# Kernel optimization log

Measured on AMD Instinct MI355X. Metric: run time of the kernel, lower is better.

The kernel has to match this reference:

```python
import jax, jax.numpy as jnp
import numpy as np

B, S, NV, D = 2, 4096, 8, 256
E = 256          # embedding dim for adaLN conditioning
H = 8            # D / n_head_channels(=32)
HID = 4 * D      # ResLayer MLP hidden
EPS = 1e-5


def setup_inputs() -> dict:
    key = jax.random.key(0)
    ks = jax.random.split(key, 16)
    M = NV * D

    def w(k, shape, scale=0.02):
        return jax.random.normal(k, shape, dtype=jnp.float32) * scale

    mask = jax.random.uniform(ks[0], (B, S, NV)) > 0.2
    mask = mask.at[..., 0].set(True)  # avoid fully-masked rows
    return {
        "x": jax.random.normal(ks[1], (B, S, NV, D), dtype=jnp.float32),
        "emb": jax.random.normal(ks[2], (B, E), dtype=jnp.float32),
        "mask": mask,
        "w_mod1": w(ks[3], (E, 2 * M)), "b_mod1": jnp.zeros((2 * M,), jnp.float32),
        "wq": w(ks[4], (D, D)), "bq": jnp.zeros((D,), jnp.float32),
        "wk": w(ks[5], (D, D)), "bk": jnp.zeros((D,), jnp.float32),
        "wv": w(ks[6], (D, D)), "bv": jnp.zeros((D,), jnp.float32),
        "wo": w(ks[7], (D, D)), "bo": jnp.zeros((D,), jnp.float32),
        "gamma": jnp.full((D,), 1e-6, jnp.float32),
        "w_mod2": w(ks[8], (E, 2 * M)), "b_mod2": jnp.zeros((2 * M,), jnp.float32),
        "w1": w(ks[9], (D, HID)), "b1": jnp.zeros((HID,), jnp.float32),
        "w2": w(ks[10], (HID, D)), "b2": jnp.zeros((D,), jnp.float32),
        "gamma_mlp": jnp.full((D,), 1e-6, jnp.float32),
    }


def _adaln(xin, emb, w, b):
    # AdaptiveLayerNorm over the flattened (NV*D) feature dims,
    # scale/shift conditioned on the embedding.
    b_, s_, nv_, d_ = xin.shape
    xf = xin.reshape(b_, s_, nv_ * d_)
    mu = xf.mean(-1, keepdims=True)
    var = ((xf - mu) ** 2).mean(-1, keepdims=True)
    normed = (xf - mu) * jax.lax.rsqrt(var + EPS)
    scale, shift = jnp.split(emb @ w + b, 2, axis=-1)  # [B, NV*D] each
    out = normed * (1.0 + scale[:, None, :]) + shift[:, None, :]
    return out.reshape(b_, s_, nv_, d_)


def reference(x, emb, mask, w_mod1, b_mod1, wq, bq, wk, bk, wv, bv, wo, bo,
              gamma, w_mod2, b_mod2, w1, b1, w2, b2, gamma_mlp):
    b_, s_, nv_, d_ = x.shape
    hd = d_ // H
    inv_sqrt = jnp.float32(1.0 / np.sqrt(hd))

    # --- attention branch: adaLN -> shape_to_att -> masked attention over variables ---
    h = _adaln(x, emb, w_mod1, b_mod1).reshape(b_ * s_, nv_, d_)
    q = (h @ wq + bq).reshape(b_ * s_, nv_, H, hd)
    k = (h @ wk + bk).reshape(b_ * s_, nv_, H, hd)
    v = (h @ wv + bv).reshape(b_ * s_, nv_, H, hd)
    scores = jnp.einsum('bnhd,bmhd->bhnm', q, k) * inv_sqrt  # [B*S, H, NV, NV]
    mk = mask.reshape(b_ * s_, nv_)
    scores = jnp.where(mk[:, None, None, :], scores, jnp.float32(-1e9))
    attn = jax.nn.softmax(scores, axis=-1)
    o = jnp.einsum('bhnm,bmhd->bnhd', attn, v).reshape(b_ * s_, nv_, d_)
    o = o @ wo + bo
    # dropout is identity at eval; gamma-scaled residual add
    x1 = x + gamma * o.reshape(b_, s_, nv_, d_)

    # --- MLP branch: shape_to_x -> adaLN -> shape_to_att -> ResLayer -> gamma residual ---
    h2 = _adaln(x1, emb, w_mod2, b_mod2)
    m = jax.nn.gelu(h2 @ w1 + b1) @ w2 + b2
    return x1 + gamma_mlp * m
```

## Files before the change

kernel.cpp:

```cpp
#include <hip/hip_runtime.h>
#include <hip/hip_bf16.h>
#include <stdint.h>

#define S_TOK   8192
#define MFEAT   2048

typedef __attribute__((ext_vector_type(4))) float f32x4;
typedef __attribute__((ext_vector_type(8))) short bf16x8;

__device__ __forceinline__ float b2f(uint32_t u) { return __uint_as_float(u << 16); }
__device__ __forceinline__ uint16_t f2b(float f) {
  uint32_t u = __float_as_uint(f);
  uint32_t r = u + 0x7fffu + ((u >> 16) & 1u);
  return (uint16_t)(r >> 16);
}

#define GLP(p) ((__attribute__((address_space(1))) void*)(uintptr_t)(p))
#define LDSP(p) ((__attribute__((address_space(3))) void*)(p))

__global__ __launch_bounds__(256) void k_maskprobe(const uint32_t* __restrict__ m,
                                                   int* __restrict__ flag) {
  __shared__ int s[5];
  const int tid = threadIdx.x;
  if (tid < 5) s[tid] = (tid == 4) ? 0 : 1;
  __syncthreads();
  bool i32ok = true, i8ok = true, f32ok = true, bf16ok = true, saw = false;
  for (int i = tid; i < 1024; i += 256) {
    uint32_t w = m[i];
    if (w > 1u) i32ok = false;
    if (((w | (w >> 8) | (w >> 16) | (w >> 24)) & 0xFEu) != 0) i8ok = false;
    if (w != 0u && w != 0x3F800000u) f32ok = false;
    uint32_t h0 = w & 0xffffu, h1 = w >> 16;
    if ((h0 != 0u && h0 != 0x3F80u) || (h1 != 0u && h1 != 0x3F80u)) bf16ok = false;
    if (w == 0x3F803F80u) saw = true;
  }
  if (!i32ok) s[0] = 0;
  if (!i8ok)  s[1] = 0;
  if (!f32ok) s[2] = 0;
  if (!bf16ok) s[3] = 0;
  if (saw)    s[4] = 1;
  __syncthreads();
  if (tid == 0) {
    int f;
    if (s[0]) f = 0;
    else if (s[1]) f = 1;
    else if (s[3] && s[4]) f = 3;
    else if (s[2]) f = 2;
    else if (s[3]) f = 3;
    else f = 0;
    *flag = f;
  }
}

__global__ __launch_bounds__(256) void k_prep(
    const float* __restrict__ wq, const float* __restrict__ wk,
    const float* __restrict__ wv, const float* __restrict__ wo,
    const float* __restrict__ w1, const float* __restrict__ w2,
    uint16_t* __restrict__ wqf, uint16_t* __restrict__ wot,
    uint16_t* __restrict__ w1f, uint16_t* __restrict__ w2f,
    const void* __restrict__ mask, const int* __restrict__ flag,
    int* __restrict__ mask_i32,
    const float* __restrict__ bq, const float* __restrict__ bk,
    const float* __restrict__ bv, float* __restrict__ biasqkv) {
  int idx = blockIdx.x * 256 + threadIdx.x;
  if (idx < 196608) {
    int o = idx, frag = o >> 9, lane = (o >> 3) & 63, sub = o & 7;
    int ct = frag >> 3, kt = frag & 7;
    int col = ct * 16 + (lane & 15);
    int k = kt * 32 + (lane >> 4) * 8 + sub;
    const float* src = (col < 256) ? wq : (col < 512) ? wk : wv;
    wqf[idx] = f2b(src[k * 256 + (col & 255)]);
  } else if (idx < 262144) {
    int r = idx - 196608;
    int k = r >> 8, n = r & 255;
    wot[n * 256 + k] = f2b(wo[r]);
  } else if (idx < 524288) {
    int o = idx - 262144, frag = o >> 9, lane = (o >> 3) & 63, sub = o & 7;
    int ct = frag >> 3, kt = frag & 7;
    int col = ct * 16 + (lane & 15);
    int k = kt * 32 + (lane >> 4) * 8 + sub;
    w1f[o] = f2b(w1[k * 1024 + col]);
  } else if (idx < 786432) {
    int o = idx - 524288, frag = o >> 9, lane = (o >> 3) & 63, sub = o & 7;
    int ct = frag >> 5, kt = frag & 31;
    int col = ct * 16 + (lane & 15);
    int k = kt * 32 + (lane >> 4) * 8 + sub;
    w2f[o] = f2b(w2[k * 256 + col]);
  } else if (idx < 851968) {
    int i = idx - 786432;
    int f = *flag;
    int v;
    if (f == 0)      v = ((const int*)mask)[i] != 0;
    else if (f == 1) v = ((const uint8_t*)mask)[i] != 0;
    else if (f == 2) v = ((const uint32_t*)mask)[i] != 0;
    else             v = ((const uint16_t*)mask)[i] != 0;
    mask_i32[i] = v;
  } else if (idx < 852736) {
    int i = idx - 851968;
    biasqkv[i] = (i < 256) ? bq[i] : (i < 512) ? bk[i - 256] : bv[i - 512];
  }
}

__global__ __launch_bounds__(256) void k_mods(
    const float* __restrict__ emb,
    const float* __restrict__ w_mod1, const float* __restrict__ b_mod1,
    const float* __restrict__ w_mod2, const float* __restrict__ b_mod2,
    float* __restrict__ mods) {
  const int j = blockIdx.x * 256 + threadIdx.x;
  const int b = blockIdx.y;
  const int which = blockIdx.z;
  const float* w  = which ? w_mod2 : w_mod1;
  const float* bb = which ? b_mod2 : b_mod1;
  __shared__ float e[256];
  e[threadIdx.x] = emb[b * 256 + threadIdx.x];
  __syncthreads();
  float acc = bb[j];
  for (int kx = 0; kx < 256; kx++) acc += e[kx] * w[(size_t)kx * 4096 + j];
  mods[((size_t)which * 2 + b) * 4096 + j] = acc;
}

__global__ __launch_bounds__(256) void k_adaln(
    const float* __restrict__ xin, const float* __restrict__ mods,
    uint16_t* __restrict__ hout, int tbase) {
  const int t = blockIdx.x;
  const int b = (tbase + t) >> 12;
  const int tid = threadIdx.x;
  const float4* xp = (const float4*)(xin + (size_t)t * MFEAT + tid * 8);
  float4 u0 = xp[0], u1 = xp[1];
  float f[8] = {u0.x, u0.y, u0.z, u0.w, u1.x, u1.y, u1.z, u1.w};
  float s1 = 0.f, s2 = 0.f;
#pragma unroll
  for (int i = 0; i < 8; i++) { s1 += f[i]; s2 += f[i] * f[i]; }
#pragma unroll
  for (int off = 32; off; off >>= 1) {
    s1 += __shfl_down(s1, off);
    s2 += __shfl_down(s2, off);
  }
  __shared__ float red[8];
  if ((tid & 63) == 0) { red[(tid >> 6) * 2] = s1; red[(tid >> 6) * 2 + 1] = s2; }
  __syncthreads();
  s1 = red[0] + red[2] + red[4] + red[6];
  s2 = red[1] + red[3] + red[5] + red[7];
  const float mean = s1 * (1.f / 2048.f);
  const float var  = s2 * (1.f / 2048.f) - mean * mean;
  const float rs = rsqrtf(var + 1e-5f);
  const float* mo = mods + (size_t)b * 4096;
  uint32_t w[4];
#pragma unroll
  for (int i = 0; i < 4; i++) {
    int j0 = tid * 8 + i * 2;
    float y0 = (f[i*2]   - mean) * rs * (1.f + mo[j0])     + mo[2048 + j0];
    float y1 = (f[i*2+1] - mean) * rs * (1.f + mo[j0 + 1]) + mo[2048 + j0 + 1];
    w[i] = (uint32_t)f2b(y0) | ((uint32_t)f2b(y1) << 16);
  }
  *(uint4*)(hout + (size_t)t * MFEAT + tid * 8) = make_uint4(w[0], w[1], w[2], w[3]);
}

template <int K, int EPI, int RESF32, int OUTF32, int SPLIT>
__global__ __launch_bounds__(256) void k_gemm(
    const uint16_t* __restrict__ A, const uint16_t* __restrict__ Wt,
    const float* __restrict__ bias, const void* res,
    const float* __restrict__ gam, void* out, int N, size_t splitStride) {
  __shared__ __align__(16) uint16_t As[128 * 64];
  __shared__ __align__(16) uint16_t Bs[128 * 64];
  const int tid = threadIdx.x;
  const int l = tid & 63;
  const int wva = tid >> 6;
  const int wr = wva >> 1, wc = wva & 1;
  const int brow = blockIdx.x * 128;
  const int bcol = blockIdx.y * 128;

  f32x4 acc[4][4];
#pragma unroll
  for (int m = 0; m < 4; m++)
#pragma unroll
    for (int n = 0; n < 4; n++) acc[m][n] = (f32x4)0.f;

  char* AsB = (char*)As;
  char* BsB = (char*)Bs;

  for (int kt = 0; kt < K / 64; ++kt) {
    const int k0 = kt * 64;
#pragma unroll
    for (int i = 0; i < 4; i++) {
      int chunk = wva * 4 + i;
      int r = chunk * 8 + (l >> 3);
      int cb = (l & 7) * 16;
      int sb = cb ^ ((r & 7) << 4);
      const uint16_t* ga = A  + (size_t)(brow + r) * K + k0 + (sb >> 1);
      const uint16_t* gb = Wt + (size_t)(bcol + r) * K + k0 + (sb >> 1);
      __builtin_amdgcn_global_load_lds(GLP(ga), LDSP(AsB + chunk * 1024), 16, 0, 0);
      __builtin_amdgcn_global_load_lds(GLP(gb), LDSP(BsB + chunk * 1024), 16, 0, 0);
    }
    asm volatile("s_waitcnt vmcnt(0)" ::: "memory");
    __syncthreads();

#pragma unroll
    for (int kk = 0; kk < 2; kk++) {
      bf16x8 a[4], b[4];
#pragma unroll
      for (int m = 0; m < 4; m++) {
        int row = wr * 64 + m * 16 + (l & 15);
        int cb = (kk * 64 + (l >> 4) * 16) ^ ((row & 7) << 4);
        a[m] = *(const bf16x8*)(AsB + row * 128 + cb);
      }
#pragma unroll
      for (int n = 0; n < 4; n++) {
        int row = wc * 64 + n * 16 + (l & 15);
        int cb = (kk * 64 + (l >> 4) * 16) ^ ((row & 7) << 4);
        b[n] = *(const bf16x8*)(BsB + row * 128 + cb);
      }
#pragma unroll
      for (int m = 0; m < 4; m++)
#pragma unroll
        for (int n = 0; n < 4; n++)
          acc[m][n] = __builtin_amdgcn_mfma_f32_16x16x32_bf16(a[m], b[n], acc[m][n], 0, 0, 0);
    }
    __syncthreads();
  }

#pragma unroll
  for (int m = 0; m < 4; m++) {
#pragma unroll
    for (int n = 0; n < 4; n++) {
      int col = bcol + wc * 64 + n * 16 + (l & 15);
      float bc = bias[col];
      float gc = (EPI == 2) ? gam[col] : 0.f;
#pragma unroll
      for (int r = 0; r < 4; r++) {
        int row = brow + wr * 64 + m * 16 + (l >> 4) * 4 + r;
        float y = acc[m][n][r] + bc;
        if (EPI == 2) {
          float rv = RESF32 ? ((const float*)res)[(size_t)row * N + col]
                            : b2f(((const uint16_t*)res)[(size_t)row * N + col]);
          y = rv + gc * y;
        }
        if (SPLIT) {
          int b_ = col >> 8, coll = col & 255;
          ((uint16_t*)out)[(size_t)b_ * splitStride + (size_t)row * 256 + coll] = f2b(y);
        } else if (OUTF32) {
          ((float*)out)[(size_t)row * N + col] = y;
        } else {
          ((uint16_t*)out)[(size_t)row * N + col] = f2b(y);
        }
      }
    }
  }
}

template <int NB>
__global__ __launch_bounds__(256) void k_panel(
    const uint16_t* __restrict__ A, const uint16_t* __restrict__ Wf,
    const float* __restrict__ bias, uint16_t* __restrict__ out,
    size_t splitStride) {
  __shared__ __align__(16) uint16_t As[128 * 256];
  const int tid = threadIdx.x;
  const int l = tid & 63;
  const int wva = tid >> 6;
  const int wr = wva >> 1, wc = wva & 1;
  const int brow = blockIdx.x * 128;
  char* AsB = (char*)As;

#pragma unroll
  for (int i = 0; i < 16; i++) {
    int chunk = wva * 16 + i;
    int r = chunk * 2 + (l >> 5);
    int sb = ((l & 31) * 16) ^ ((r & 7) << 4);
    __builtin_amdgcn_global_load_lds(GLP(A + (size_t)(brow + r) * 256 + (sb >> 1)),
                                     LDSP(AsB + chunk * 1024), 16, 0, 0);
  }
  asm volatile("s_waitcnt vmcnt(0)" ::: "memory");
  __syncthreads();

#pragma unroll 1
  for (int nb = 0; nb < NB; nb++) {
    f32x4 acc[4][4];
#pragma unroll
    for (int m = 0; m < 4; m++)
#pragma unroll
      for (int n = 0; n < 4; n++) acc[m][n] = (f32x4)0.f;

#pragma unroll
    for (int kt = 0; kt < 8; kt++) {
      bf16x8 a[4], b[4];
#pragma unroll
      for (int n = 0; n < 4; n++) {
        int ct = nb * 8 + wc * 4 + n;
        b[n] = *(const bf16x8*)(Wf + (((size_t)ct * 8 + kt) * 64 + l) * 8);
      }
#pragma unroll
      for (int m = 0; m < 4; m++) {
        int row = wr * 64 + m * 16 + (l & 15);
        int cb = (kt * 64 + (l >> 4) * 16) ^ ((row & 7) << 4);
        a[m] = *(const bf16x8*)(AsB + row * 512 + cb);
      }
#pragma unroll
      for (int m = 0; m < 4; m++)
#pragma unroll
        for (int n = 0; n < 4; n++)
          acc[m][n] = __builtin_amdgcn_mfma_f32_16x16x32_bf16(a[m], b[n], acc[m][n], 0, 0, 0);
    }

#pragma unroll
    for (int m = 0; m < 4; m++) {
#pragma unroll
      for (int n = 0; n < 4; n++) {
        int col = nb * 128 + wc * 64 + n * 16 + (l & 15);
        float bc = bias[col];
        int b_ = col >> 8, coll = col & 255;
#pragma unroll
        for (int r = 0; r < 4; r++) {
          int row = brow + wr * 64 + m * 16 + (l >> 4) * 4 + r;
          out[(size_t)b_ * splitStride + (size_t)row * 256 + coll] = f2b(acc[m][n][r] + bc);
        }
      }
    }
  }
}

__global__ __launch_bounds__(256) void k_mlp(
    const uint16_t* __restrict__ A, const uint16_t* __restrict__ w1f,
    const float* __restrict__ b1, const uint16_t* __restrict__ w2f,
    const float* __restrict__ b2, const float* __restrict__ gam,
    float* x1c) {
  __shared__ __align__(16) uint16_t As[64 * 256];
  __shared__ __align__(16) uint16_t Hs[64 * 128];
  const int tid = threadIdx.x;
  const int l = tid & 63;
  const int w = tid >> 6;
  const int brow = blockIdx.x * 64;
  char* AsB = (char*)As;
  char* HsB = (char*)Hs;

#pragma unroll
  for (int i = 0; i < 8; i++) {
    int chunk = w * 8 + i;
    int r = chunk * 2 + (l >> 5);
    int sb = ((l & 31) * 16) ^ ((r & 7) << 4);
    __builtin_amdgcn_global_load_lds(GLP(A + (size_t)(brow + r) * 256 + (sb >> 1)),
                                     LDSP(AsB + chunk * 1024), 16, 0, 0);
  }

  f32x4 acc2[4][4];
#pragma unroll
  for (int m = 0; m < 4; m++)
#pragma unroll
    for (int n = 0; n < 4; n++) acc2[m][n] = (f32x4)0.f;

  asm volatile("s_waitcnt vmcnt(0)" ::: "memory");
  __syncthreads();

#pragma unroll 1
  for (int c = 0; c < 8; c++) {
    f32x4 acc1[2][4];
#pragma unroll
    for (int n = 0; n < 2; n++)
#pragma unroll
      for (int m = 0; m < 4; m++) acc1[n][m] = (f32x4)0.f;
#pragma unroll
    for (int kt = 0; kt < 8; kt++) {
      bf16x8 a[4], b[2];
#pragma unroll
      for (int n = 0; n < 2; n++) {
        int ct = c * 8 + w * 2 + n;
        b[n] = *(const bf16x8*)(w1f + (((size_t)ct * 8 + kt) * 64 + l) * 8);
      }
#pragma unroll
      for (int m = 0; m < 4; m++) {
        int row = m * 16 + (l & 15);
        int cb = (kt * 64 + (l >> 4) * 16) ^ ((row & 7) << 4);
        a[m] = *(const bf16x8*)(AsB + row * 512 + cb);
      }
#pragma unroll
      for (int n = 0; n < 2; n++)
#pragma unroll
        for (int m = 0; m < 4; m++)
          acc1[n][m] = __builtin_amdgcn_mfma_f32_16x16x32_bf16(b[n], a[m], acc1[n][m], 0, 0, 0);
    }
    __syncthreads();
#pragma unroll
    for (int n = 0; n < 2; n++) {
      int hb = w * 32 + n * 16 + (l >> 4) * 4;
      float4 bb = *(const float4*)(b1 + c * 128 + hb);
#pragma unroll
      for (int m = 0; m < 4; m++) {
        int token = m * 16 + (l & 15);
        uint32_t pk[2];
#pragma unroll
        for (int h = 0; h < 2; h++) {
          float g[2];
#pragma unroll
          for (int j = 0; j < 2; j++) {
            float y = acc1[n][m][h * 2 + j] + ((const float*)&bb)[h * 2 + j];
            g[j] = y / (1.f + __expf(-1.702f * y));
          }
          pk[h] = (uint32_t)f2b(g[0]) | ((uint32_t)f2b(g[1]) << 16);
        }
        int byte = (token * 256 + hb * 2) ^ ((token & 7) << 4);
        *(uint2*)(HsB + byte) = make_uint2(pk[0], pk[1]);
      }
    }
    __syncthreads();
#pragma unroll
    for (int kt = 0; kt < 4; kt++) {
      bf16x8 h[4], b[4];
#pragma unroll
      for (int n = 0; n < 4; n++) {
        int ct = w * 4 + n;
        int kidx = c * 4 + kt;
        b[n] = *(const bf16x8*)(w2f + (((size_t)ct * 32 + kidx) * 64 + l) * 8);
      }
#pragma unroll
      for (int m = 0; m < 4; m++) {
        int row = m * 16 + (l & 15);
        int cb = (kt * 64 + (l >> 4) * 16) ^ ((row & 7) << 4);
        h[m] = *(const bf16x8*)(HsB + row * 256 + cb);
      }
#pragma unroll
      for (int m = 0; m < 4; m++)
#pragma unroll
        for (int n = 0; n < 4; n++)
          acc2[m][n] = __builtin_amdgcn_mfma_f32_16x16x32_bf16(h[m], b[n], acc2[m][n], 0, 0, 0);
    }
  }

#pragma unroll
  for (int m = 0; m < 4; m++) {
#pragma unroll
    for (int n = 0; n < 4; n++) {
      int col = w * 64 + n * 16 + (l & 15);
      float bc = b2[col];
      float gc = gam[col];
#pragma unroll
      for (int r = 0; r < 4; r++) {
        int row = brow + m * 16 + (l >> 4) * 4 + r;
        float y = x1c[(size_t)row * 256 + col] + gc * (acc2[m][n][r] + bc);
        x1c[(size_t)row * 256 + col] = y;
      }
    }
  }
}

__global__ __launch_bounds__(256) void k_attn(
    const uint16_t* __restrict__ q, const uint16_t* __restrict__ k,
    const uint16_t* __restrict__ v, const int* __restrict__ mask,
    uint16_t* __restrict__ o) {
  __shared__ __align__(16) uint16_t kk[4][2048];
  __shared__ __align__(16) uint16_t vv[4][2048];
  const int l = threadIdx.x & 63;
  const int wva = threadIdx.x >> 6;
  const int t = blockIdx.x * 4 + wva;

#pragma unroll
  for (int c = 0; c < 4; c++) {
    __builtin_amdgcn_global_load_lds(GLP(k + (size_t)t * 2048 + c * 512 + l * 8),
                                     LDSP(&kk[wva][c * 512]), 16, 0, 0);
    __builtin_amdgcn_global_load_lds(GLP(v + (size_t)t * 2048 + c * 512 + l * 8),
                                     LDSP(&vv[wva][c * 512]), 16, 0, 0);
  }

  const int h = l >> 3, n = l & 7;
  const uint4* qp = (const uint4*)(q + (size_t)t * 2048 + n * 256 + h * 32);
  float qf[32];
#pragma unroll
  for (int c = 0; c < 4; c++) {
    uint4 u = qp[c];
    qf[c*8+0]=b2f(u.x & 0xffff); qf[c*8+1]=b2f(u.x >> 16);
    qf[c*8+2]=b2f(u.y & 0xffff); qf[c*8+3]=b2f(u.y >> 16);
    qf[c*8+4]=b2f(u.z & 0xffff); qf[c*8+5]=b2f(u.z >> 16);
    qf[c*8+6]=b2f(u.w & 0xffff); qf[c*8+7]=b2f(u.w >> 16);
  }
  asm volatile("s_waitcnt vmcnt(0)" ::: "memory");

  float s[8];
#pragma unroll
  for (int m = 0; m < 8; m++) {
    const uint4* kp = (const uint4*)&kk[wva][m * 256 + h * 32];
    float acc = 0.f;
#pragma unroll
    for (int c = 0; c < 4; c++) {
      uint4 u = kp[c];
      acc += qf[c*8+0]*b2f(u.x & 0xffff) + qf[c*8+1]*b2f(u.x >> 16)
           + qf[c*8+2]*b2f(u.y & 0xffff) + qf[c*8+3]*b2f(u.y >> 16)
           + qf[c*8+4]*b2f(u.z & 0xffff) + qf[c*8+5]*b2f(u.z >> 16)
           + qf[c*8+6]*b2f(u.w & 0xffff) + qf[c*8+7]*b2f(u.w >> 16);
    }
    s[m] = acc * 0.17677669529663687f;
  }
  const int* mk = mask + (size_t)t * 8;
  float mx = -1e30f;
#pragma unroll
  for (int m = 0; m < 8; m++) { s[m] = mk[m] ? s[m] : -1e9f; mx = fmaxf(mx, s[m]); }
  float p[8], sum = 0.f;
#pragma unroll
  for (int m = 0; m < 8; m++) { p[m] = __expf(s[m] - mx); sum += p[m]; }
  float inv = 1.f / sum;
  float of[32];
#pragma unroll
  for (int d = 0; d < 32; d++) of[d] = 0.f;
#pragma unroll
  for (int m = 0; m < 8; m++) {
    float pm = p[m] * inv;
    const uint4* vp = (const uint4*)&vv[wva][m * 256 + h * 32];
#pragma unroll
    for (int c = 0; c < 4; c++) {
      uint4 u = vp[c];
      of[c*8+0]+=pm*b2f(u.x & 0xffff); of[c*8+1]+=pm*b2f(u.x >> 16);
      of[c*8+2]+=pm*b2f(u.y & 0xffff); of[c*8+3]+=pm*b2f(u.y >> 16);
      of[c*8+4]+=pm*b2f(u.z & 0xffff); of[c*8+5]+=pm*b2f(u.z >> 16);
      of[c*8+6]+=pm*b2f(u.w & 0xffff); of[c*8+7]+=pm*b2f(u.w >> 16);
    }
  }
  uint16_t* op = o + (size_t)t * 2048 + n * 256 + h * 32;
#pragma unroll
  for (int c = 0; c < 4; c++) {
    uint32_t w0 = (uint32_t)f2b(of[c*8+0]) | ((uint32_t)f2b(of[c*8+1]) << 16);
    uint32_t w1 = (uint32_t)f2b(of[c*8+2]) | ((uint32_t)f2b(of[c*8+3]) << 16);
    uint32_t w2 = (uint32_t)f2b(of[c*8+4]) | ((uint32_t)f2b(of[c*8+5]) << 16);
    uint32_t w3 = (uint32_t)f2b(of[c*8+6]) | ((uint32_t)f2b(of[c*8+7]) << 16);
    ((uint4*)op)[c] = make_uint4(w0, w1, w2, w3);
  }
}

extern "C" void kernel_launch(void* const* d_in, const int* in_sizes, int n_in,
                              void* d_out, int out_size, void* d_ws, size_t ws_size,
                              hipStream_t stream) {
  const float* x      = (const float*)d_in[0];
  const float* emb    = (const float*)d_in[1];
  const void*  mask   = d_in[2];
  const float* w_mod1 = (const float*)d_in[3];
  const float* b_mod1 = (const float*)d_in[4];
  const float* wq = (const float*)d_in[5];
  const float* bq = (const float*)d_in[6];
  const float* wk = (const float*)d_in[7];
  const float* bk = (const float*)d_in[8];
  const float* wv = (const float*)d_in[9];
  const float* bv = (const float*)d_in[10];
  const float* wo = (const float*)d_in[11];
  const float* bo = (const float*)d_in[12];
  const float* gamma     = (const float*)d_in[13];
  const float* w_mod2    = (const float*)d_in[14];
  const float* b_mod2    = (const float*)d_in[15];
  const float* w1 = (const float*)d_in[16];
  const float* b1 = (const float*)d_in[17];
  const float* w2 = (const float*)d_in[18];
  const float* b2 = (const float*)d_in[19];
  const float* gamma_mlp = (const float*)d_in[20];

  char* ws = (char*)d_ws;
  float*    mods = (float*)ws;
  uint16_t* wqf = (uint16_t*)(ws + 65536);
  uint16_t* wot = wqf + 196608;
  uint16_t* w1f = wot + 65536;
  uint16_t* w2f = w1f + 262144;
  int*      mask_i32 = (int*)(w2f + 262144);
  int*      flag = mask_i32 + 65536;
  float*    biasqkv = (float*)(flag + 1);
  uint16_t* slots = (uint16_t*)(ws + (2u << 20));
  float*    xout = (float*)d_out;

  size_t budget = (ws_size > (3u << 20)) ? ws_size - (2u << 20) : 0;
  int maxtok = (int)(budget / 16384);
  int chunk_tokens = 16;
  for (int c = 8192; c >= 16; c >>= 1) { if (c <= maxtok) { chunk_tokens = c; break; } }
  const int nchunks = S_TOK / chunk_tokens;
  const int crows = chunk_tokens * 8;
  const size_t slot = (size_t)crows * 256;
  uint16_t* C0 = slots;
  uint16_t* C1 = C0 + slot;

  k_maskprobe<<<dim3(1), 256, 0, stream>>>((const uint32_t*)mask, flag);
  k_prep<<<dim3(3331), 256, 0, stream>>>(wq, wk, wv, wo, w1, w2, wqf, wot, w1f, w2f,
                                         mask, flag, mask_i32, bq, bk, bv, biasqkv);
  k_mods<<<dim3(16, 2, 2), 256, 0, stream>>>(emb, w_mod1, b_mod1, w_mod2, b_mod2, mods);

  for (int c = 0; c < nchunks; c++) {
    const int t0 = c * chunk_tokens;
    const size_t eo = (size_t)t0 * MFEAT;
    const float* xc = x + eo;
    float* x1c = xout + eo;
    k_adaln<<<dim3(chunk_tokens), 256, 0, stream>>>(xc, mods, C0, t0);
    k_panel<6><<<dim3(crows / 128), 256, 0, stream>>>(C0, wqf, biasqkv, C1, slot);
    k_attn<<<dim3(chunk_tokens / 4), 256, 0, stream>>>(C1, C1 + slot, C1 + 2 * slot,
                                                       mask_i32 + (size_t)t0 * 8, C0);
    k_gemm<256, 2, 1, 1, 0><<<dim3(crows / 128, 2), 256, 0, stream>>>(
        C0, wot, bo, xc, gamma, x1c, 256, 0);
    k_adaln<<<dim3(chunk_tokens), 256, 0, stream>>>(x1c, mods + 2 * 4096, C0, t0);
    k_mlp<<<dim3(crows / 64), 256, 0, stream>>>(C0, w1f, b1, w2f, b2, gamma_mlp, x1c);
  }
}
```

Measured before the change: 335.6 us.

## Fuse adaLN into QKV and MLP GEMMs, convert o-proj to fragment-layout panel

Removes the two standalone adaLN kernels by computing per-token mean/variance and the modulated normalization inside the QKV projection and MLP kernels, writing bf16 directly into LDS. This cuts the intermediate bf16 activation round-trip through global memory and two launches per chunk. The output projection switches from a tiled LDS GEMM with transposed weights to a panel kernel reading pre-fragmented weights. The cost is that x rows are read twice inside each fused kernel (once for stats, once for normalization), and the extra reductions add shared-memory work.

```diff
diff --git a/kernel.cpp b/kernel.cpp
--- a/kernel.cpp
+++ b/kernel.cpp
@@ -56,7 +56,7 @@
     const float* __restrict__ wq, const float* __restrict__ wk,
     const float* __restrict__ wv, const float* __restrict__ wo,
     const float* __restrict__ w1, const float* __restrict__ w2,
-    uint16_t* __restrict__ wqf, uint16_t* __restrict__ wot,
+    uint16_t* __restrict__ wqf, uint16_t* __restrict__ wof,
     uint16_t* __restrict__ w1f, uint16_t* __restrict__ w2f,
     const void* __restrict__ mask, const int* __restrict__ flag,
     int* __restrict__ mask_i32,
@@ -71,9 +71,11 @@
     const float* src = (col < 256) ? wq : (col < 512) ? wk : wv;
     wqf[idx] = f2b(src[k * 256 + (col & 255)]);
   } else if (idx < 262144) {
-    int r = idx - 196608;
-    int k = r >> 8, n = r & 255;
-    wot[n * 256 + k] = f2b(wo[r]);
+    int o = idx - 196608, frag = o >> 9, lane = (o >> 3) & 63, sub = o & 7;
+    int ct = frag >> 3, kt = frag & 7;
+    int col = ct * 16 + (lane & 15);
+    int k = kt * 32 + (lane >> 4) * 8 + sub;
+    wof[o] = f2b(wo[k * 256 + col]);
   } else if (idx < 524288) {
     int o = idx - 262144, frag = o >> 9, lane = (o >> 3) & 63, sub = o & 7;
     int ct = frag >> 3, kt = frag & 7;
@@ -119,96 +121,93 @@
   mods[((size_t)which * 2 + b) * 4096 + j] = acc;
 }
 
-__global__ __launch_bounds__(256) void k_adaln(
-    const float* __restrict__ xin, const float* __restrict__ mods,
-    uint16_t* __restrict__ hout, int tbase) {
-  const int t = blockIdx.x;
-  const int b = (tbase + t) >> 12;
-  const int tid = threadIdx.x;
-  const float4* xp = (const float4*)(xin + (size_t)t * MFEAT + tid * 8);
-  float4 u0 = xp[0], u1 = xp[1];
-  float f[8] = {u0.x, u0.y, u0.z, u0.w, u1.x, u1.y, u1.z, u1.w};
-  float s1 = 0.f, s2 = 0.f;
-#pragma unroll
-  for (int i = 0; i < 8; i++) { s1 += f[i]; s2 += f[i] * f[i]; }
-#pragma unroll
-  for (int off = 32; off; off >>= 1) {
-    s1 += __shfl_down(s1, off);
-    s2 += __shfl_down(s2, off);
-  }
-  __shared__ float red[8];
-  if ((tid & 63) == 0) { red[(tid >> 6) * 2] = s1; red[(tid >> 6) * 2 + 1] = s2; }
-  __syncthreads();
-  s1 = red[0] + red[2] + red[4] + red[6];
-  s2 = red[1] + red[3] + red[5] + red[7];
-  const float mean = s1 * (1.f / 2048.f);
-  const float var  = s2 * (1.f / 2048.f) - mean * mean;
-  const float rs = rsqrtf(var + 1e-5f);
-  const float* mo = mods + (size_t)b * 4096;
-  uint32_t w[4];
-#pragma unroll
-  for (int i = 0; i < 4; i++) {
-    int j0 = tid * 8 + i * 2;
-    float y0 = (f[i*2]   - mean) * rs * (1.f + mo[j0])     + mo[2048 + j0];
-    float y1 = (f[i*2+1] - mean) * rs * (1.f + mo[j0 + 1]) + mo[2048 + j0 + 1];
-    w[i] = (uint32_t)f2b(y0) | ((uint32_t)f2b(y1) << 16);
-  }
-  *(uint4*)(hout + (size_t)t * MFEAT + tid * 8) = make_uint4(w[0], w[1], w[2], w[3]);
-}
-
-template <int K, int EPI, int RESF32, int OUTF32, int SPLIT>
-__global__ __launch_bounds__(256) void k_gemm(
-    const uint16_t* __restrict__ A, const uint16_t* __restrict__ Wt,
-    const float* __restrict__ bias, const void* res,
-    const float* __restrict__ gam, void* out, int N, size_t splitStride) {
-  __shared__ __align__(16) uint16_t As[128 * 64];
-  __shared__ __align__(16) uint16_t Bs[128 * 64];
+__global__ __launch_bounds__(256) void k_qkv(
+    const float* __restrict__ x, const float* __restrict__ mods,
+    const float* __restrict__ biasqkv, const uint16_t* __restrict__ wqf,
+    uint16_t* __restrict__ out, size_t slot, int t0) {
+  __shared__ __align__(16) uint16_t As[128 * 256];
+  __shared__ float red1[256], red2[256];
   const int tid = threadIdx.x;
   const int l = tid & 63;
   const int wva = tid >> 6;
   const int wr = wva >> 1, wc = wva & 1;
   const int brow = blockIdx.x * 128;
-  const int bcol = blockIdx.y * 128;
-
-  f32x4 acc[4][4];
-#pragma unroll
-  for (int m = 0; m < 4; m++)
-#pragma unroll
-    for (int n = 0; n < 4; n++) acc[m][n] = (f32x4)0.f;
-
   char* AsB = (char*)As;
-  char* BsB = (char*)Bs;
-
-  for (int kt = 0; kt < K / 64; ++kt) {
-    const int k0 = kt * 64;
+
+  {
+    const int r = tid >> 1, ch = (tid & 1) << 7;
+    const float4* xp = (const float4*)(x + (size_t)(brow + r) * 256 + ch);
+    float s1 = 0.f, s2 = 0.f;
+#pragma unroll
+    for (int i = 0; i < 32; i++) {
+      float4 u = xp[i];
+      s1 += u.x + u.y + u.z + u.w;
+      s2 += u.x * u.x + u.y * u.y + u.z * u.z + u.w * u.w;
+    }
+    red1[tid] = s1; red2[tid] = s2;
+  }
+  __syncthreads();
+  {
+    const int r = tid >> 1;
+    const int base = (r >> 3) << 4;
+    float s1 = 0.f, s2 = 0.f;
+#pragma unroll
+    for (int i = 0; i < 16; i++) { s1 += red1[base + i]; s2 += red2[base + i]; }
+    float mean = s1 * (1.f / 2048.f);
+    float var = s2 * (1.f / 2048.f) - mean * mean;
+    float rs = rsqrtf(var + 1e-5f);
+    __syncthreads();
+    red1[r] = mean; red2[r] = rs;
+  }
+  __syncthreads();
+
+#pragma unroll
+  for (int it = 0; it < 16; it++) {
+    int cidx = it * 256 + tid;
+    int row = cidx >> 5, cg = cidx & 31;
+    int b = (t0 + ((brow + row) >> 3)) >> 12;
+    const float* mo = mods + (size_t)b * 4096 + ((row & 7) << 8) + cg * 8;
+    float mean = red1[row], rs = red2[row];
+    const float4* xp = (const float4*)(x + (size_t)(brow + row) * 256 + cg * 8);
+    float4 u0 = xp[0], u1 = xp[1];
+    float4 c0 = *(const float4*)mo,        c1 = *(const float4*)(mo + 4);
+    float4 h0 = *(const float4*)(mo + 2048), h1 = *(const float4*)(mo + 2052);
+    float v[8] = {u0.x,u0.y,u0.z,u0.w,u1.x,u1.y,u1.z,u1.w};
+    float sc[8] = {c0.x,c0.y,c0.z,c0.w,c1.x,c1.y,c1.z,c1.w};
+    float sh[8] = {h0.x,h0.y,h0.z,h0.w,h1.x,h1.y,h1.z,h1.w};
+    uint32_t w[4];
 #pragma unroll
     for (int i = 0; i < 4; i++) {
-      int chunk = wva * 4 + i;
-      int r = chunk * 8 + (l >> 3);
-      int cb = (l & 7) * 16;
-      int sb = cb ^ ((r & 7) << 4);
-      const uint16_t* ga = A  + (size_t)(brow + r) * K + k0 + (sb >> 1);
-      const uint16_t* gb = Wt + (size_t)(bcol + r) * K + k0 + (sb >> 1);
-      __builtin_amdgcn_global_load_lds(GLP(ga), LDSP(AsB + chunk * 1024), 16, 0, 0);
-      __builtin_amdgcn_global_load_lds(GLP(gb), LDSP(BsB + chunk * 1024), 16, 0, 0);
-    }
-    asm volatile("s_waitcnt vmcnt(0)" ::: "memory");
-    __syncthreads();
-
-#pragma unroll
-    for (int kk = 0; kk < 2; kk++) {
+      float y0 = (v[i*2]   - mean) * rs * (1.f + sc[i*2])   + sh[i*2];
+      float y1 = (v[i*2+1] - mean) * rs * (1.f + sc[i*2+1]) + sh[i*2+1];
+      w[i] = (uint32_t)f2b(y0) | ((uint32_t)f2b(y1) << 16);
+    }
+    *(uint4*)(AsB + row * 512 + ((cg * 16) ^ ((row & 7) << 4))) =
+        make_uint4(w[0], w[1], w[2], w[3]);
+  }
+  __syncthreads();
+
+#pragma unroll 1
+  for (int nb = 0; nb < 6; nb++) {
+    f32x4 acc[4][4];
+#pragma unroll
+    for (int m = 0; m < 4; m++)
+#pragma unroll
+      for (int n = 0; n < 4; n++) acc[m][n] = (f32x4)0.f;
+
+#pragma unroll
+    for (int kt = 0; kt < 8; kt++) {
       bf16x8 a[4], b[4];
+#pragma unroll
+      for (int n = 0; n < 4; n++) {
+        int ct = nb * 8 + wc * 4 + n;
+        b[n] = *(const bf16x8*)(wqf + (((size_t)ct * 8 + kt) * 64 + l) * 8);
+      }
 #pragma unroll
       for (int m = 0; m < 4; m++) {
         int row = wr * 64 + m * 16 + (l & 15);
-        int cb = (kk * 64 + (l >> 4) * 16) ^ ((row & 7) << 4);
-        a[m] = *(const bf16x8*)(AsB + row * 128 + cb);
-      }
-#pragma unroll
-      for (int n = 0; n < 4; n++) {
-        int row = wc * 64 + n * 16 + (l & 15);
-        int cb = (kk * 64 + (l >> 4) * 16) ^ ((row & 7) << 4);
-        b[n] = *(const bf16x8*)(BsB + row * 128 + cb);
+        int cb = (kt * 64 + (l >> 4) * 16) ^ ((row & 7) << 4);
+        a[m] = *(const bf16x8*)(AsB + row * 512 + cb);
       }
 #pragma unroll
       for (int m = 0; m < 4; m++)
@@ -216,43 +215,28 @@
         for (int n = 0; n < 4; n++)
           acc[m][n] = __builtin_amdgcn_mfma_f32_16x16x32_bf16(a[m], b[n], acc[m][n], 0, 0, 0);
     }
-    __syncthreads();
-  }
-
-#pragma unroll
-  for (int m = 0; m < 4; m++) {
-#pragma unroll
-    for (int n = 0; n < 4; n++) {
-      int col = bcol + wc * 64 + n * 16 + (l & 15);
-      float bc = bias[col];
-      float gc = (EPI == 2) ? gam[col] : 0.f;
-#pragma unroll
-      for (int r = 0; r < 4; r++) {
-        int row = brow + wr * 64 + m * 16 + (l >> 4) * 4 + r;
-        float y = acc[m][n][r] + bc;
-        if (EPI == 2) {
-          float rv = RESF32 ? ((const float*)res)[(size_t)row * N + col]
-                            : b2f(((const uint16_t*)res)[(size_t)row * N + col]);
-          y = rv + gc * y;
+
+#pragma unroll
+    for (int m = 0; m < 4; m++) {
+#pragma unroll
+      for (int n = 0; n < 4; n++) {
+        int col = nb * 128 + wc * 64 + n * 16 + (l & 15);
+        float bc = biasqkv[col];
+        int b_ = col >> 8, coll = col & 255;
+#pragma unroll
+        for (int r = 0; r < 4; r++) {
+          int row = brow + wr * 64 + m * 16 + (l >> 4) * 4 + r;
+          out[(size_t)b_ * slot + (size_t)row * 256 + coll] = f2b(acc[m][n][r] + bc);
         }
-        if (SPLIT) {
-          int b_ = col >> 8, coll = col & 255;
-          ((uint16_t*)out)[(size_t)b_ * splitStride + (size_t)row * 256 + coll] = f2b(y);
-        } else if (OUTF32) {
-          ((float*)out)[(size_t)row * N + col] = y;
-        } else {
-          ((uint16_t*)out)[(size_t)row * N + col] = f2b(y);
-        }
-      }
-    }
-  }
-}
-
-template <int NB>
-__global__ __launch_bounds__(256) void k_panel(
-    const uint16_t* __restrict__ A, const uint16_t* __restrict__ Wf,
-    const float* __restrict__ bias, uint16_t* __restrict__ out,
-    size_t splitStride) {
+      }
+    }
+  }
+}
+
+__global__ __launch_bounds__(256) void k_oproj(
+    const uint16_t* __restrict__ A, const uint16_t* __restrict__ wof,
+    const float* __restrict__ bias, const float* __restrict__ res,
+    const float* __restrict__ gam, float* __restrict__ out) {
   __shared__ __align__(16) uint16_t As[128 * 256];
   const int tid = threadIdx.x;
   const int l = tid & 63;
@@ -273,7 +257,7 @@
   __syncthreads();
 
 #pragma unroll 1
-  for (int nb = 0; nb < NB; nb++) {
+  for (int nb = 0; nb < 2; nb++) {
     f32x4 acc[4][4];
 #pragma unroll
     for (int m = 0; m < 4; m++)
@@ -286,7 +270,7 @@
 #pragma unroll
       for (int n = 0; n < 4; n++) {
         int ct = nb * 8 + wc * 4 + n;
-        b[n] = *(const bf16x8*)(Wf + (((size_t)ct * 8 + kt) * 64 + l) * 8);
+        b[n] = *(const bf16x8*)(wof + (((size_t)ct * 8 + kt) * 64 + l) * 8);
       }
 #pragma unroll
       for (int m = 0; m < 4; m++) {
@@ -307,11 +291,12 @@
       for (int n = 0; n < 4; n++) {
         int col = nb * 128 + wc * 64 + n * 16 + (l & 15);
         float bc = bias[col];
-        int b_ = col >> 8, coll = col & 255;
+        float gc = gam[col];
 #pragma unroll
         for (int r = 0; r < 4; r++) {
           int row = brow + wr * 64 + m * 16 + (l >> 4) * 4 + r;
-          out[(size_t)b_ * splitStride + (size_t)row * 256 + coll] = f2b(acc[m][n][r] + bc);
+          out[(size_t)row * 256 + col] =
+              res[(size_t)row * 256 + col] + gc * (acc[m][n][r] + bc);
         }
       }
     }
@@ -319,12 +304,13 @@
 }
 
 __global__ __launch_bounds__(256) void k_mlp(
-    const uint16_t* __restrict__ A, const uint16_t* __restrict__ w1f,
-    const float* __restrict__ b1, const uint16_t* __restrict__ w2f,
-    const float* __restrict__ b2, const float* __restrict__ gam,
-    float* x1c) {
+    float* x1c, const float* __restrict__ mods,
+    const uint16_t* __restrict__ w1f, const float* __restrict__ b1,
+    const uint16_t* __restrict__ w2f, const float* __restrict__ b2,
+    const float* __restrict__ gam, int t0) {
   __shared__ __align__(16) uint16_t As[64 * 256];
   __shared__ __align__(16) uint16_t Hs[64 * 128];
+  __shared__ float red1[256], red2[256];
   const int tid = threadIdx.x;
   const int l = tid & 63;
   const int w = tid >> 6;
@@ -332,13 +318,56 @@
   char* AsB = (char*)As;
   char* HsB = (char*)Hs;
 
-#pragma unroll
-  for (int i = 0; i < 8; i++) {
-    int chunk = w * 8 + i;
-    int r = chunk * 2 + (l >> 5);
-    int sb = ((l & 31) * 16) ^ ((r & 7) << 4);
-    __builtin_amdgcn_global_load_lds(GLP(A + (size_t)(brow + r) * 256 + (sb >> 1)),
-                                     LDSP(AsB + chunk * 1024), 16, 0, 0);
+  {
+    const int r = tid >> 2, q = (tid & 3) << 6;
+    const float4* xp = (const float4*)(x1c + (size_t)(brow + r) * 256 + q);
+    float s1 = 0.f, s2 = 0.f;
+#pragma unroll
+    for (int i = 0; i < 16; i++) {
+      float4 u = xp[i];
+      s1 += u.x + u.y + u.z + u.w;
+      s2 += u.x * u.x + u.y * u.y + u.z * u.z + u.w * u.w;
+    }
+    red1[tid] = s1; red2[tid] = s2;
+  }
+  __syncthreads();
+  {
+    const int r = tid >> 2;
+    const int base = (r >> 3) << 5;
+    float s1 = 0.f, s2 = 0.f;
+#pragma unroll
+    for (int i = 0; i < 32; i++) { s1 += red1[base + i]; s2 += red2[base + i]; }
+    float mean = s1 * (1.f / 2048.f);
+    float var = s2 * (1.f / 2048.f) - mean * mean;
+    float rs = rsqrtf(var + 1e-5f);
+    __syncthreads();
+    red1[r] = mean; red2[r] = rs;
+  }
+  __syncthreads();
+
+#pragma unroll
+  for (int it = 0; it < 8; it++) {
+    int cidx = it * 256 + tid;
+    int row = cidx >> 5, cg = cidx & 31;
+    int b = (t0 + ((brow + row) >> 3)) >> 12;
+    const float* mo = mods + (size_t)b * 4096 + ((row & 7) << 8) + cg * 8;
+    float mean = red1[row], rs = red2[row];
+    const float4* xp = (const float4*)(x1c + (size_t)(brow + row) * 256 + cg * 8);
+    float4 u0 = xp[0], u1 = xp[1];
+    float4 c0 = *(const float4*)mo,        c1 = *(const float4*)(mo + 4);
+    float4 h0 = *(const float4*)(mo + 2048), h1 = *(const float4*)(mo + 2052);
+    float v[8] = {u0.x,u0.y,u0.z,u0.w,u1.x,u1.y,u1.z,u1.w};
+    float sc[8] = {c0.x,c0.y,c0.z,c0.w,c1.x,c1.y,c1.z,c1.w};
+    float sh[8] = {h0.x,h0.y,h0.z,h0.w,h1.x,h1.y,h1.z,h1.w};
+    uint32_t wv[4];
+#pragma unroll
+    for (int i = 0; i < 4; i++) {
+      float y0 = (v[i*2]   - mean) * rs * (1.f + sc[i*2])   + sh[i*2];
+      float y1 = (v[i*2+1] - mean) * rs * (1.f + sc[i*2+1]) + sh[i*2+1];
+      wv[i] = (uint32_t)f2b(y0) | ((uint32_t)f2b(y1) << 16);
+    }
+    *(uint4*)(AsB + row * 512 + ((cg * 16) ^ ((row & 7) << 4))) =
+        make_uint4(wv[0], wv[1], wv[2], wv[3]);
   }
 
   f32x4 acc2[4][4];
@@ -346,8 +375,6 @@
   for (int m = 0; m < 4; m++)
 #pragma unroll
     for (int n = 0; n < 4; n++) acc2[m][n] = (f32x4)0.f;
-
-  asm volatile("s_waitcnt vmcnt(0)" ::: "memory");
   __syncthreads();
 
 #pragma unroll 1
@@ -550,8 +577,8 @@
   char* ws = (char*)d_ws;
   float*    mods = (float*)ws;
   uint16_t* wqf = (uint16_t*)(ws + 65536);
-  uint16_t* wot = wqf + 196608;
-  uint16_t* w1f = wot + 65536;
+  uint16_t* wof = wqf + 196608;
+  uint16_t* w1f = wof + 65536;
   uint16_t* w2f = w1f + 262144;
   int*      mask_i32 = (int*)(w2f + 262144);
   int*      flag = mask_i32 + 65536;
@@ -570,7 +597,7 @@
   uint16_t* C1 = C0 + slot;
 
   k_maskprobe<<<dim3(1), 256, 0, stream>>>((const uint32_t*)mask, flag);
-  k_prep<<<dim3(3331), 256, 0, stream>>>(wq, wk, wv, wo, w1, w2, wqf, wot, w1f, w2f,
+  k_prep<<<dim3(3331), 256, 0, stream>>>(wq, wk, wv, wo, w1, w2, wqf, wof, w1f, w2f,
                                          mask, flag, mask_i32, bq, bk, bv, biasqkv);
   k_mods<<<dim3(16, 2, 2), 256, 0, stream>>>(emb, w_mod1, b_mod1, w_mod2, b_mod2, mods);
 
@@ -579,13 +606,11 @@
     const size_t eo = (size_t)t0 * MFEAT;
     const float* xc = x + eo;
     float* x1c = xout + eo;
-    k_adaln<<<dim3(chunk_tokens), 256, 0, stream>>>(xc, mods, C0, t0);
-    k_panel<6><<<dim3(crows / 128), 256, 0, stream>>>(C0, wqf, biasqkv, C1, slot);
+    k_qkv<<<dim3(crows / 128), 256, 0, stream>>>(xc, mods, biasqkv, wqf, C1, slot, t0);
     k_attn<<<dim3(chunk_tokens / 4), 256, 0, stream>>>(C1, C1 + slot, C1 + 2 * slot,
                                                        mask_i32 + (size_t)t0 * 8, C0);
-    k_gemm<256, 2, 1, 1, 0><<<dim3(crows / 128, 2), 256, 0, stream>>>(
-        C0, wot, bo, xc, gamma, x1c, 256, 0);
-    k_adaln<<<dim3(chunk_tokens), 256, 0, stream>>>(x1c, mods + 2 * 4096, C0, t0);
-    k_mlp<<<dim3(crows / 64), 256, 0, stream>>>(C0, w1f, b1, w2f, b2, gamma_mlp, x1c);
-  }
-}
+    k_oproj<<<dim3(crows / 128), 256, 0, stream>>>(C0, wof, bo, xc, gamma, x1c);
+    k_mlp<<<dim3(crows / 64), 256, 0, stream>>>(x1c, mods + 2 * 4096, w1f, b1,
+                                                w2f, b2, gamma_mlp, t0);
+  }
+}
```

Measured after the change: 347.2 us. 3.5% more time.
